# Kernel optimization log

Hardware: AMD Instinct MI355X
Metric: run time of the kernel (lower is better)

The kernel has to match this reference:

```python
import jax, jax.numpy as jnp
import numpy as np
import math

HEAD_SIZE = 64
BN_EPS = 1e-5  # BatchNorm eval with default running stats (mean=0, var=1)


def _rope_tables(seq_len, d):
    pos = jnp.arange(seq_len, dtype=jnp.float32)[:, None]
    div = jnp.exp(jnp.arange(0, d, 2, dtype=jnp.float32) * (-math.log(10000.0) / d))
    cos_pos = jnp.repeat(jnp.cos(pos * div), 2, axis=-1)  # [n, d]
    sin_pos = jnp.repeat(jnp.sin(pos * div), 2, axis=-1)  # [n, d]
    return cos_pos, sin_pos


def _rope(x, cos_pos, sin_pos):
    # interleaved rotation: (x0,x1) -> (-x1, x0)
    x2 = jnp.stack([-x[..., 1::2], x[..., ::2]], axis=-1).reshape(x.shape)
    return x * cos_pos + x2 * sin_pos


def _cbam(x, mlp_w1, mlp_b1, mlp_w2, mlp_b2, conv_w):
    # Channel gate: shared MLP over avg- and max-pooled [b, c] descriptors
    def mlp(v):
        return jax.nn.relu(v @ mlp_w1 + mlp_b1) @ mlp_w2 + mlp_b2
    avg = x.mean(axis=(2, 3))
    mx = x.max(axis=(2, 3))
    scale = jax.nn.sigmoid(mlp(avg) + mlp(mx))[:, :, None, None]
    x = x * scale
    # Spatial gate: 7x7 conv over channel-pooled (max, mean) maps
    comp = jnp.stack([x.max(axis=1), x.mean(axis=1)], axis=1)  # [b, 2, m, n]
    conv = jax.lax.conv_general_dilated(
        comp, conv_w, window_strides=(1, 1), padding=[(3, 3), (3, 3)],
        dimension_numbers=('NCHW', 'OIHW', 'NCHW'))
    conv = conv / jnp.sqrt(jnp.float32(1.0 + BN_EPS))  # identity BatchNorm (eval)
    return x * jax.nn.sigmoid(conv)


def setup_inputs() -> dict:
    key = jax.random.key(0)
    ks = jax.random.split(key, 12)
    b, n, h, c, d = 2, 512, 768, 108, HEAD_SIZE
    s = 0.02
    return {
        'inputs': jax.random.normal(ks[0], (b, n, h), jnp.float32),
        'event_inputs': jax.random.normal(ks[1], (c, h), jnp.float32),
        'mask': jnp.ones((b, n), jnp.int32),
        'w_dense': jax.random.normal(ks[2], (h, 2 * d), jnp.float32) * s,
        'b_dense': jax.random.normal(ks[3], (2 * d,), jnp.float32) * s,
        'w_event': jax.random.normal(ks[4], (h, d), jnp.float32) * s,
        'b_event': jax.random.normal(ks[5], (d,), jnp.float32) * s,
        'mlp_w1': jax.random.normal(ks[6], (c, c // 16), jnp.float32) * s,
        'mlp_b1': jax.random.normal(ks[7], (c // 16,), jnp.float32) * s,
        'mlp_w2': jax.random.normal(ks[8], (c // 16, c), jnp.float32) * s,
        'mlp_b2': jax.random.normal(ks[9], (c,), jnp.float32) * s,
        'conv_w': jax.random.normal(ks[10], (1, 2, 7, 7), jnp.float32) * s,
    }


def reference(inputs, event_inputs, mask, w_dense, b_dense, w_event, b_event,
              mlp_w1, mlp_b1, mlp_w2, mlp_b2, conv_w):
    b, n, _ = inputs.shape
    seq = inputs @ w_dense + b_dense          # [b, n, 2*d]
    ev = event_inputs @ w_event + b_event     # [c, d]
    qw, kw = seq[..., :HEAD_SIZE], seq[..., HEAD_SIZE:]
    cos_pos, sin_pos = _rope_tables(n, HEAD_SIZE)
    qw = _rope(qw, cos_pos, sin_pos)
    kw = _rope(kw, cos_pos, sin_pos)
    # event_output is broadcast over batch, so bcd collapses to cd
    logits = jnp.einsum('bmd,bnd,cd->bcmn', qw, kw, ev)
    logits = _cbam(logits, mlp_w1, mlp_b1, mlp_w2, mlp_b2, conv_w) + logits
    pad = (1 - mask).astype(bool)
    neg_inf = jnp.float32(-jnp.inf)
    logits = jnp.where(pad[:, None, :, None], neg_inf, logits)
    logits = jnp.where(pad[:, None, None, :], neg_inf, logits)
    tril_pen = jnp.tril(jnp.ones((n, n), logits.dtype), -1) * jnp.float32(1e12)
    logits = logits - tril_pen
    return logits / (HEAD_SIZE ** 0.5)
```

## Files before the change

kernel.cpp:

```cpp
#include <hip/hip_runtime.h>

constexpr int nB = 2;
constexpr int nS = 512;
constexpr int nH = 768;
constexpr int nC = 108;
constexpr int nD = 64;
constexpr int nBC = nB * nC;
constexpr long long nSS = (long long)nS * nS;

constexpr size_t QW_OFF    = 0;
constexpr size_t KW_OFF    = QW_OFF + (size_t)nB*nS*nD;
constexpr size_t EV_OFF    = KW_OFF + (size_t)nB*nS*nD;
constexpr size_t SUM_OFF   = EV_OFF + (size_t)nC*nD;
constexpr size_t MAX_OFF   = SUM_OFF + nBC;
constexpr size_t SCALE_OFF = MAX_OFF + nBC;
constexpr size_t COMP_OFF  = SCALE_OFF + nBC;
constexpr size_t SIG_OFF   = COMP_OFF + (size_t)nB*2*nS*nS;

typedef __attribute__((ext_vector_type(8))) short short8;
typedef __attribute__((ext_vector_type(4))) float f32x4;
union UFrag { uint4 u; short8 s; };

__device__ inline void atomicMaxF(float* addr, float v) {
    if (v >= 0.f) atomicMax((int*)addr, __float_as_int(v));
    else          atomicMin((unsigned int*)addr, __float_as_uint(v));
}

__device__ inline unsigned pack2bf(float a, float b) {
    unsigned ua = __float_as_uint(a), ub = __float_as_uint(b);
    ua = (ua + 0x7FFFu + ((ua >> 16) & 1u)) >> 16;
    ub = (ub + 0x7FFFu + ((ub >> 16) & 1u)) >> 16;
    return ua | (ub << 16);
}

__global__ __launch_bounds__(128) void k1_proj(
    const float* __restrict__ in, const float* __restrict__ evin,
    const float* __restrict__ wd, const float* __restrict__ bd,
    const float* __restrict__ we, const float* __restrict__ be,
    float* __restrict__ ws)
{
    __shared__ float rowS[nH];
    __shared__ float seqS[128];
    const int blk = blockIdx.x, tid = threadIdx.x;
    if (blk == 0 && tid < nBC) { ws[SUM_OFF + tid] = 0.f; ws[MAX_OFF + tid] = -INFINITY; }
    if (blk < nB * nS) {
        const int b = blk >> 9, m = blk & 511;
        const float* row = in + (size_t)blk * nH;
        for (int k = tid; k < nH; k += 128) rowS[k] = row[k];
        __syncthreads();
        float acc = bd[tid];
        for (int k = 0; k < nH; ++k) acc += rowS[k] * wd[k * 128 + tid];
        seqS[tid] = acc;
        __syncthreads();
        const int half = tid >> 6;
        const int j = tid & 63;
        const int p = j >> 1;
        const float div = expf(-0.28782313662425572f * (float)p);
        const float ang = (float)m * div;
        const float c = cosf(ang), s = sinf(ang);
        const float x0 = seqS[half * 64 + (j & ~1)];
        const float x1 = seqS[half * 64 + (j | 1)];
        const float v = (j & 1) ? (x1 * c + x0 * s) : (x0 * c - x1 * s);
        const size_t off = (half ? KW_OFF : QW_OFF) + ((size_t)(b * nS + m)) * nD + j;
        ws[off] = v;
    } else {
        const int ci = blk - nB * nS;
        const float* row = evin + (size_t)ci * nH;
        for (int k = tid; k < nH; k += 128) rowS[k] = row[k];
        __syncthreads();
        if (tid < nD) {
            float acc = be[tid];
            for (int k = 0; k < nH; ++k) acc += rowS[k] * we[k * nD + tid];
            ws[EV_OFF + (size_t)ci * nD + tid] = acc;
        }
    }
}


__device__ inline void stage_ev(const float* __restrict__ ws, uint4* evS, int tid) {
    for (int idx = tid; idx < 112 * 8; idx += 256) {
        const int row = idx >> 3, g = idx & 7;
        uint4 u = make_uint4(0, 0, 0, 0);
        if (row < nC) {
            const float* ep = ws + EV_OFF + row * nD + g * 8;
            float4 a = *(const float4*)ep;
            float4 b = *(const float4*)(ep + 4);
            u.x = pack2bf(a.x, a.y); u.y = pack2bf(a.z, a.w);
            u.z = pack2bf(b.x, b.y); u.w = pack2bf(b.z, b.w);
        }
        evS[row * 8 + (g ^ (row & 7))] = u;
    }
}

__device__ inline void stage_qk(const float* __restrict__ ws, float (*qkS)[68],
                                int b, int m0, int n0, int tid) {
    for (int idx = tid; idx < 64 * 16; idx += 256) {
        const int row = idx >> 4, d4 = (idx & 15) * 4;
        const float* src = (row < 32)
            ? (ws + QW_OFF + ((size_t)(b * nS + m0 + row)) * nD + d4)
            : (ws + KW_OFF + ((size_t)(b * nS + n0 + (row - 32))) * nD + d4);
        const float4 v = *(const float4*)src;
        qkS[row][d4 + 0] = v.x; qkS[row][d4 + 1] = v.y;
        qkS[row][d4 + 2] = v.z; qkS[row][d4 + 3] = v.w;
    }
}

__device__ inline void build_U(const float (*qkS)[68], uint4* U, int si, int sj, int tid) {
    const float* qr = qkS[si * 16 + (tid >> 4)];
    const float* kr = qkS[32 + sj * 16 + (tid & 15)];
#pragma unroll
    for (int g = 0; g < 8; ++g) {
        uint4 u;
        u.x = pack2bf(qr[g*8+0]*kr[g*8+0], qr[g*8+1]*kr[g*8+1]);
        u.y = pack2bf(qr[g*8+2]*kr[g*8+2], qr[g*8+3]*kr[g*8+3]);
        u.z = pack2bf(qr[g*8+4]*kr[g*8+4], qr[g*8+5]*kr[g*8+5]);
        u.w = pack2bf(qr[g*8+6]*kr[g*8+6], qr[g*8+7]*kr[g*8+7]);
        U[tid * 8 + (g ^ (tid & 7))] = u;
    }
}

__global__ __launch_bounds__(256) void kS_stats(float* __restrict__ ws)
{
    __shared__ uint4 evS[112 * 8];
    __shared__ uint4 U[256 * 8];
    __shared__ float qkS[64][68];
    __shared__ float sS[4][112], mS[4][112];

    const int tid = threadIdx.x;
    const int b = blockIdx.y;
    const int m0 = (blockIdx.x >> 4) * 32, n0 = (blockIdx.x & 15) * 32;
    const int lane = tid & 63, w = tid >> 6;
    const int fr = lane & 15, fg = lane >> 4;

    stage_ev(ws, evS, tid);
    stage_qk(ws, qkS, b, m0, n0, tid);

    float psum[28], pmax[28];
#pragma unroll
    for (int i = 0; i < 28; ++i) { psum[i] = 0.f; pmax[i] = -INFINITY; }

    for (int st = 0; st < 4; ++st) {
        __syncthreads();
        build_U(qkS, U, st >> 1, st & 1, tid);
        __syncthreads();

        short8 uf[4][2];
#pragma unroll
        for (int nf = 0; nf < 4; ++nf)
#pragma unroll
            for (int ks = 0; ks < 2; ++ks) {
                const int row = w * 64 + nf * 16 + fr;
                UFrag u; u.u = U[row * 8 + ((ks * 4 + fg) ^ (row & 7))];
                uf[nf][ks] = u.s;
            }
#pragma unroll
        for (int cf = 0; cf < 7; ++cf) {
            short8 ef[2];
#pragma unroll
            for (int ks = 0; ks < 2; ++ks) {
                const int row = cf * 16 + fr;
                UFrag u; u.u = evS[row * 8 + ((ks * 4 + fg) ^ (row & 7))];
                ef[ks] = u.s;
            }
            f32x4 acc[4] = {};
#pragma unroll
            for (int ks = 0; ks < 2; ++ks)
#pragma unroll
                for (int nf = 0; nf < 4; ++nf)
                    acc[nf] = __builtin_amdgcn_mfma_f32_16x16x32_bf16(ef[ks], uf[nf][ks], acc[nf], 0, 0, 0);
#pragma unroll
            for (int nf = 0; nf < 4; ++nf)
#pragma unroll
                for (int r = 0; r < 4; ++r) {
                    const float v = acc[nf][r];
                    psum[cf * 4 + r] += v;
                    pmax[cf * 4 + r] = fmaxf(pmax[cf * 4 + r], v);
                }
        }
    }

#pragma unroll
    for (int i = 0; i < 28; ++i) {
#pragma unroll
        for (int off = 1; off < 16; off <<= 1) {
            psum[i] += __shfl_xor(psum[i], off, 64);
            pmax[i] = fmaxf(pmax[i], __shfl_xor(pmax[i], off, 64));
        }
    }
    if (fr == 0) {
#pragma unroll
        for (int cf = 0; cf < 7; ++cf)
#pragma unroll
            for (int r = 0; r < 4; ++r) {
                const int c = cf * 16 + fg * 4 + r;
                sS[w][c] = psum[cf * 4 + r];
                mS[w][c] = pmax[cf * 4 + r];
            }
    }
    __syncthreads();
    if (tid < nC) {
        const float s = sS[0][tid] + sS[1][tid] + sS[2][tid] + sS[3][tid];
        const float mx = fmaxf(fmaxf(mS[0][tid], mS[1][tid]), fmaxf(mS[2][tid], mS[3][tid]));
        atomicAdd(&ws[SUM_OFF + b * nC + tid], s);
        atomicMaxF(&ws[MAX_OFF + b * nC + tid], mx);
    }
}

__global__ __launch_bounds__(256) void kC_comp(
    float* __restrict__ ws, const float* __restrict__ w1, const float* __restrict__ b1,
    const float* __restrict__ w2, const float* __restrict__ b2)
{
    __shared__ uint4 evS[112 * 8];
    __shared__ uint4 U[256 * 8];
    __shared__ float qkS[64][68];
    __shared__ float hS[12], scS[112];

    const int tid = threadIdx.x;
    const int b = blockIdx.y;
    const int m0 = (blockIdx.x >> 4) * 32, n0 = (blockIdx.x & 15) * 32;
    const int lane = tid & 63, w = tid >> 6;
    const int fr = lane & 15, fg = lane >> 4;

    if (tid < 12) {
        const int src = tid / 6, j = tid % 6;
        const float* v = ws + (src ? MAX_OFF : SUM_OFF) + b * nC;
        const float sc = src ? 1.f : (1.f / (float)nSS);
        float acc = b1[j];
        for (int cc = 0; cc < nC; ++cc) acc += v[cc] * sc * w1[cc * 6 + j];
        hS[tid] = fmaxf(acc, 0.f);
    }
    stage_ev(ws, evS, tid);
    stage_qk(ws, qkS, b, m0, n0, tid);
    __syncthreads();
    if (tid < 112) {
        float s = 0.f;
        if (tid < nC) {
            float acc = 2.f * b2[tid];
#pragma unroll
            for (int j = 0; j < 6; ++j) acc += (hS[j] + hS[6 + j]) * w2[j * nC + tid];
            s = 1.f / (1.f + expf(-acc));
            if (blockIdx.x == 0) ws[SCALE_OFF + b * nC + tid] = s;
        }
        scS[tid] = s;
    }

    for (int st = 0; st < 4; ++st) {
        const int si = st >> 1, sj = st & 1;
        __syncthreads();
        build_U(qkS, U, si, sj, tid);
        __syncthreads();

        short8 uf[4][2];
#pragma unroll
        for (int nf = 0; nf < 4; ++nf)
#pragma unroll
            for (int ks = 0; ks < 2; ++ks) {
                const int row = w * 64 + nf * 16 + fr;
                UFrag u; u.u = U[row * 8 + ((ks * 4 + fg) ^ (row & 7))];
                uf[nf][ks] = u.s;
            }
        float mx[4], sm[4];
#pragma unroll
        for (int nf = 0; nf < 4; ++nf) { mx[nf] = -INFINITY; sm[nf] = 0.f; }
#pragma unroll
        for (int cf = 0; cf < 7; ++cf) {
            short8 ef[2];
#pragma unroll
            for (int ks = 0; ks < 2; ++ks) {
                const int row = cf * 16 + fr;
                UFrag u; u.u = evS[row * 8 + ((ks * 4 + fg) ^ (row & 7))];
                ef[ks] = u.s;
            }
            f32x4 acc[4] = {};
#pragma unroll
            for (int ks = 0; ks < 2; ++ks)
#pragma unroll
                for (int nf = 0; nf < 4; ++nf)
                    acc[nf] = __builtin_amdgcn_mfma_f32_16x16x32_bf16(ef[ks], uf[nf][ks], acc[nf], 0, 0, 0);
            const bool valid = (cf < 6) || (fg < 3);
#pragma unroll
            for (int nf = 0; nf < 4; ++nf)
#pragma unroll
                for (int r = 0; r < 4; ++r) {
                    const float v = scS[cf * 16 + fg * 4 + r] * acc[nf][r];
                    sm[nf] += v;
                    if (valid) mx[nf] = fmaxf(mx[nf], v);
                }
        }
#pragma unroll
        for (int nf = 0; nf < 4; ++nf) {
            mx[nf] = fmaxf(mx[nf], __shfl_xor(mx[nf], 16, 64));
            mx[nf] = fmaxf(mx[nf], __shfl_xor(mx[nf], 32, 64));
            sm[nf] += __shfl_xor(sm[nf], 16, 64);
            sm[nf] += __shfl_xor(sm[nf], 32, 64);
        }
        if (fg == 0) {
#pragma unroll
            for (int nf = 0; nf < 4; ++nf) {
                const int m = m0 + si * 16 + 4 * w + nf;
                const int n = n0 + sj * 16 + fr;
                ws[COMP_OFF + (((size_t)(b * 2 + 0)) * nS + m) * nS + n] = mx[nf];
                ws[COMP_OFF + (((size_t)(b * 2 + 1)) * nS + m) * nS + n] = sm[nf] * (1.f / (float)nC);
            }
        }
    }
}

__global__ __launch_bounds__(512) void k5_conv(float* __restrict__ ws, const float* __restrict__ cw)
{
    __shared__ float S[14][520];
    __shared__ float wS[98];
    const int n = threadIdx.x;
    const int m = blockIdx.x & 511;
    const int b = blockIdx.x >> 9;
    if (n < 98) wS[n] = cw[n];
    for (int idx = n; idx < 14 * 518; idx += 512) {
        const int col = idx % 518;
        const int r = idx / 518;
        const int ch = r / 7, ky = r % 7;
        const int y = m + ky - 3;
        const int x = col - 3;
        float v = 0.f;
        if (y >= 0 && y < nS && x >= 0 && x < nS)
            v = ws[COMP_OFF + (((size_t)(b * 2 + ch)) * nS + y) * nS + x];
        S[r][col] = v;
    }
    __syncthreads();
    float acc = 0.f;
#pragma unroll
    for (int r = 0; r < 14; ++r)
#pragma unroll
        for (int kx = 0; kx < 7; ++kx)
            acc += S[r][n + kx] * wS[r * 7 + kx];
    acc *= 0.9999950000374997f;
    ws[SIG_OFF + ((size_t)b * nS + m) * nS + n] = 1.f / (1.f + expf(-acc));
}

__device__ inline void stage_tiles(const float* qwp, const float* kwp, const float* evp,
                                   uint4* ldsA, uint4* ldsB, int tid)
{
#pragma unroll
    for (int i = 0; i < 4; ++i) {
        const int q = tid + i * 256;
        const int row = q >> 3, g = q & 7;
        const int sw = row * 8 + (g ^ (row & 7));
        float4 x0 = *(const float4*)(qwp + row * nD + g * 8);
        float4 x1 = *(const float4*)(qwp + row * nD + g * 8 + 4);
        float4 e0 = *(const float4*)(evp + g * 8);
        float4 e1 = *(const float4*)(evp + g * 8 + 4);
        uint4 w;
        w.x = pack2bf(x0.x * e0.x, x0.y * e0.y);
        w.y = pack2bf(x0.z * e0.z, x0.w * e0.w);
        w.z = pack2bf(x1.x * e1.x, x1.y * e1.y);
        w.w = pack2bf(x1.z * e1.z, x1.w * e1.w);
        ldsA[sw] = w;
        float4 y0 = *(const float4*)(kwp + row * nD + g * 8);
        float4 y1 = *(const float4*)(kwp + row * nD + g * 8 + 4);
        uint4 v;
        v.x = pack2bf(y0.x, y0.y);
        v.y = pack2bf(y0.z, y0.w);
        v.z = pack2bf(y1.x, y1.y);
        v.w = pack2bf(y1.z, y1.w);
        ldsB[sw] = v;
    }
}

__device__ inline void mfma_tile(const uint4* ldsA, const uint4* ldsB,
                                 int wr, int wc, int fr, int fg, f32x4 acc[4][4])
{
#pragma unroll
    for (int ks = 0; ks < 2; ++ks) {
        short8 kf[4], qf[4];
#pragma unroll
        for (int i = 0; i < 4; ++i) {
            const int row = wc * 64 + i * 16 + fr;
            const int g = ks * 4 + fg;
            UFrag u; u.u = ldsB[row * 8 + (g ^ (row & 7))];
            kf[i] = u.s;
        }
#pragma unroll
        for (int j = 0; j < 4; ++j) {
            const int row = wr * 64 + j * 16 + fr;
            const int g = ks * 4 + fg;
            UFrag u; u.u = ldsA[row * 8 + (g ^ (row & 7))];
            qf[j] = u.s;
        }
#pragma unroll
        for (int i = 0; i < 4; ++i)
#pragma unroll
            for (int j = 0; j < 4; ++j)
                acc[i][j] = __builtin_amdgcn_mfma_f32_16x16x32_bf16(kf[i], qf[j], acc[i][j], 0, 0, 0);
    }
}

__global__ __launch_bounds__(256) void k6_final(
    float* __restrict__ ws, float* __restrict__ out, const int* __restrict__ mask)
{
    __shared__ uint4 ldsA[128 * 8];
    __shared__ uint4 ldsB[128 * 8];

    const int tid = threadIdx.x;
    const int mt = blockIdx.x >> 2, nt = blockIdx.x & 3;
    const int c  = blockIdx.y;
    const int b  = blockIdx.z;
    const int m0 = mt * 128, n0 = nt * 128;

    stage_tiles(ws + QW_OFF + ((size_t)(b * nS + m0)) * nD,
                ws + KW_OFF + ((size_t)(b * nS + n0)) * nD,
                ws + EV_OFF + (size_t)c * nD, ldsA, ldsB, tid);
    __syncthreads();

    const int lane = tid & 63;
    const int wv = tid >> 6;
    const int wr = wv >> 1, wc = wv & 1;
    const int fr = lane & 15, fg = lane >> 4;

    f32x4 acc[4][4] = {};
    mfma_tile(ldsA, ldsB, wr, wc, fr, fg, acc);

    const float scale = ws[SCALE_OFF + b * nC + c];
    const float* sig = ws + SIG_OFF + (size_t)b * nS * nS;
    float* outb = out + (size_t)(b * nC + c) * nSS;

#pragma unroll
    for (int i = 0; i < 4; ++i) {
#pragma unroll
        for (int j = 0; j < 4; ++j) {
            const int m = m0 + wr * 64 + j * 16 + fr;
            const int nb = n0 + wc * 64 + i * 16 + fg * 4;
            const float4 sg = *(const float4*)(sig + (size_t)m * nS + nb);
            const int mrow = mask[b * nS + m];
            const int4 mcol = *(const int4*)(mask + b * nS + nb);
            const f32x4 a = acc[i][j];
            float r[4];
            const float sgv[4] = { sg.x, sg.y, sg.z, sg.w };
            const int mcv[4] = { mcol.x, mcol.y, mcol.z, mcol.w };
#pragma unroll
            for (int rr = 0; rr < 4; ++rr) {
                float v = a[rr] * (1.f + scale * sgv[rr]);
                if (!mrow || !mcv[rr]) v = -INFINITY;
                if (m > nb + rr) v -= 1e12f;
                r[rr] = v * 0.125f;
            }
            *(float4*)(outb + (size_t)m * nS + nb) = make_float4(r[0], r[1], r[2], r[3]);
        }
    }
}

extern "C" void kernel_launch(void* const* d_in, const int* in_sizes, int n_in,
                              void* d_out, int out_size, void* d_ws, size_t ws_size,
                              hipStream_t stream)
{
    const float* inputs = (const float*)d_in[0];
    const float* evin   = (const float*)d_in[1];
    const int*   mask   = (const int*)d_in[2];
    const float* wd     = (const float*)d_in[3];
    const float* bd     = (const float*)d_in[4];
    const float* we     = (const float*)d_in[5];
    const float* be     = (const float*)d_in[6];
    const float* w1     = (const float*)d_in[7];
    const float* b1     = (const float*)d_in[8];
    const float* w2     = (const float*)d_in[9];
    const float* b2     = (const float*)d_in[10];
    const float* cw     = (const float*)d_in[11];
    float* out = (float*)d_out;
    float* ws  = (float*)d_ws;

    k1_proj<<<nB * nS + nC, 128, 0, stream>>>(inputs, evin, wd, bd, we, be, ws);
    kS_stats<<<dim3(256, nB), 256, 0, stream>>>(ws);
    kC_comp<<<dim3(256, nB), 256, 0, stream>>>(ws, w1, b1, w2, b2);
    k5_conv<<<nB * nS, 512, 0, stream>>>(ws, cw);
    k6_final<<<dim3(16, nC, nB), 256, 0, stream>>>(ws, out, mask);
}
```

Before: 172.2 us.

## Compute channel means algebraically and skip tril-masked tiles in conv and final

The channel average of the trilinear logits is now computed in closed form, as ev dotted with the product of summed q and k rows. The stats kernel therefore only tracks the max. The projection kernel now handles four rows per block and accumulates those q/k column sums atomically. The comp, conv and final kernels skip tiles strictly below the diagonal, where the 1e12 penalty dominates, and the final kernel writes a constant there. That constant drops CBAM terms which are negligible against the penalty, so it depends on float rounding of the huge offset.

New measurement: 170.1 us. Within noise of the previous version (-1.2%).

```diff
diff --git a/kernel.cpp b/kernel.cpp
--- a/kernel.cpp
+++ b/kernel.cpp
@@ -11,11 +11,11 @@
 constexpr size_t QW_OFF    = 0;
 constexpr size_t KW_OFF    = QW_OFF + (size_t)nB*nS*nD;
 constexpr size_t EV_OFF    = KW_OFF + (size_t)nB*nS*nD;
-constexpr size_t SUM_OFF   = EV_OFF + (size_t)nC*nD;
-constexpr size_t MAX_OFF   = SUM_OFF + nBC;
+constexpr size_t MAX_OFF   = EV_OFF + (size_t)nC*nD;
 constexpr size_t SCALE_OFF = MAX_OFF + nBC;
 constexpr size_t COMP_OFF  = SCALE_OFF + nBC;
 constexpr size_t SIG_OFF   = COMP_OFF + (size_t)nB*2*nS*nS;
+constexpr size_t SQK_OFF   = SIG_OFF;
 
 typedef __attribute__((ext_vector_type(8))) short short8;
 typedef __attribute__((ext_vector_type(4))) float f32x4;
@@ -33,49 +33,76 @@
     return ua | (ub << 16);
 }
 
-__global__ __launch_bounds__(128) void k1_proj(
+__global__ __launch_bounds__(256) void k1_proj(
     const float* __restrict__ in, const float* __restrict__ evin,
     const float* __restrict__ wd, const float* __restrict__ bd,
     const float* __restrict__ we, const float* __restrict__ be,
     float* __restrict__ ws)
 {
-    __shared__ float rowS[nH];
-    __shared__ float seqS[128];
+    __shared__ float rowT[nH][4];
+    __shared__ float accS[2][4][128];
+    __shared__ float ropeS[2][4][64];
     const int blk = blockIdx.x, tid = threadIdx.x;
-    if (blk == 0 && tid < nBC) { ws[SUM_OFF + tid] = 0.f; ws[MAX_OFF + tid] = -INFINITY; }
-    if (blk < nB * nS) {
-        const int b = blk >> 9, m = blk & 511;
-        const float* row = in + (size_t)blk * nH;
-        for (int k = tid; k < nH; k += 128) rowS[k] = row[k];
-        __syncthreads();
-        float acc = bd[tid];
-        for (int k = 0; k < nH; ++k) acc += rowS[k] * wd[k * 128 + tid];
-        seqS[tid] = acc;
-        __syncthreads();
-        const int half = tid >> 6;
-        const int j = tid & 63;
+    if (blk == 0 && tid < nBC) ws[MAX_OFF + tid] = -INFINITY;
+    if (blk < 256) {
+        const int b = blk >> 7;
+        const int m0 = (blk & 127) << 2;
+        const float* src = in + ((size_t)(b * nS + m0)) * nH;
+        for (int q = tid; q < 4 * nH; q += 256) {
+            const int r = q / nH, k = q - r * nH;
+            rowT[k][r] = src[q];
+        }
+        __syncthreads();
+        const int h = tid >> 7, c = tid & 127;
+        float a0 = h ? 0.f : bd[c], a1 = 0.f, a2 = 0.f, a3 = 0.f;
+        const float* wp = wd + (size_t)(h * 384) * 128 + c;
+        for (int k = h * 384; k < h * 384 + 384; ++k, wp += 128) {
+            const float w = *wp;
+            const float4 rv = *(const float4*)&rowT[k][0];
+            a0 += rv.x * w; a1 += rv.y * w; a2 += rv.z * w; a3 += rv.w * w;
+        }
+        accS[h][0][c] = a0; accS[h][1][c] = a1; accS[h][2][c] = a2; accS[h][3][c] = a3;
+        __syncthreads();
+        const int r = tid >> 6, j = tid & 63;
+        const int m = m0 + r;
         const int p = j >> 1;
         const float div = expf(-0.28782313662425572f * (float)p);
         const float ang = (float)m * div;
-        const float c = cosf(ang), s = sinf(ang);
-        const float x0 = seqS[half * 64 + (j & ~1)];
-        const float x1 = seqS[half * 64 + (j | 1)];
-        const float v = (j & 1) ? (x1 * c + x0 * s) : (x0 * c - x1 * s);
-        const size_t off = (half ? KW_OFF : QW_OFF) + ((size_t)(b * nS + m)) * nD + j;
-        ws[off] = v;
+        const float co = cosf(ang), si = sinf(ang);
+#pragma unroll
+        for (int half = 0; half < 2; ++half) {
+            const int i0 = half * 64 + (j & ~1);
+            const int i1 = half * 64 + (j | 1);
+            const float x0 = accS[0][r][i0] + accS[1][r][i0];
+            const float x1 = accS[0][r][i1] + accS[1][r][i1];
+            const float v = (j & 1) ? (x1 * co + x0 * si) : (x0 * co - x1 * si);
+            ws[(half ? KW_OFF : QW_OFF) + ((size_t)(b * nS + m)) * nD + j] = v;
+            ropeS[half][r][j] = v;
+        }
+        __syncthreads();
+        if (tid < 128) {
+            const int half = tid >> 6, jj = tid & 63;
+            const float t = ropeS[half][0][jj] + ropeS[half][1][jj]
+                          + ropeS[half][2][jj] + ropeS[half][3][jj];
+            atomicAdd(&ws[SQK_OFF + b * 128 + half * 64 + jj], t);
+        }
     } else {
-        const int ci = blk - nB * nS;
-        const float* row = evin + (size_t)ci * nH;
-        for (int k = tid; k < nH; k += 128) rowS[k] = row[k];
+        const int ci = blk - 256;
+        float* evrow = &rowT[0][0];
+        for (int k = tid; k < nH; k += 256) evrow[k] = evin[(size_t)ci * nH + k];
+        __syncthreads();
+        const int c = tid & 63, h = tid >> 6;
+        float acc = 0.f;
+        for (int k = h * 192; k < h * 192 + 192; ++k) acc += evrow[k] * we[k * nD + c];
+        accS[0][h][c] = acc;
         __syncthreads();
         if (tid < nD) {
-            float acc = be[tid];
-            for (int k = 0; k < nH; ++k) acc += rowS[k] * we[k * nD + tid];
-            ws[EV_OFF + (size_t)ci * nD + tid] = acc;
-        }
-    }
-}
-
+            const float s = be[tid] + accS[0][0][tid] + accS[0][1][tid]
+                          + accS[0][2][tid] + accS[0][3][tid];
+            ws[EV_OFF + (size_t)ci * nD + tid] = s;
+        }
+    }
+}
 
 __device__ inline void stage_ev(const float* __restrict__ ws, uint4* evS, int tid) {
     for (int idx = tid; idx < 112 * 8; idx += 256) {
@@ -124,7 +151,7 @@
     __shared__ uint4 evS[112 * 8];
     __shared__ uint4 U[256 * 8];
     __shared__ float qkS[64][68];
-    __shared__ float sS[4][112], mS[4][112];
+    __shared__ float mS[4][112];
 
     const int tid = threadIdx.x;
     const int b = blockIdx.y;
@@ -135,9 +162,9 @@
     stage_ev(ws, evS, tid);
     stage_qk(ws, qkS, b, m0, n0, tid);
 
-    float psum[28], pmax[28];
-#pragma unroll
-    for (int i = 0; i < 28; ++i) { psum[i] = 0.f; pmax[i] = -INFINITY; }
+    float pmax[28];
+#pragma unroll
+    for (int i = 0; i < 28; ++i) pmax[i] = -INFINITY;
 
     for (int st = 0; st < 4; ++st) {
         __syncthreads();
@@ -171,37 +198,27 @@
 #pragma unroll
             for (int nf = 0; nf < 4; ++nf)
 #pragma unroll
-                for (int r = 0; r < 4; ++r) {
-                    const float v = acc[nf][r];
-                    psum[cf * 4 + r] += v;
-                    pmax[cf * 4 + r] = fmaxf(pmax[cf * 4 + r], v);
-                }
+                for (int r = 0; r < 4; ++r)
+                    pmax[cf * 4 + r] = fmaxf(pmax[cf * 4 + r], acc[nf][r]);
         }
     }
 
 #pragma unroll
     for (int i = 0; i < 28; ++i) {
 #pragma unroll
-        for (int off = 1; off < 16; off <<= 1) {
-            psum[i] += __shfl_xor(psum[i], off, 64);
+        for (int off = 1; off < 16; off <<= 1)
             pmax[i] = fmaxf(pmax[i], __shfl_xor(pmax[i], off, 64));
-        }
     }
     if (fr == 0) {
 #pragma unroll
         for (int cf = 0; cf < 7; ++cf)
 #pragma unroll
-            for (int r = 0; r < 4; ++r) {
-                const int c = cf * 16 + fg * 4 + r;
-                sS[w][c] = psum[cf * 4 + r];
-                mS[w][c] = pmax[cf * 4 + r];
-            }
+            for (int r = 0; r < 4; ++r)
+                mS[w][cf * 16 + fg * 4 + r] = pmax[cf * 4 + r];
     }
     __syncthreads();
     if (tid < nC) {
-        const float s = sS[0][tid] + sS[1][tid] + sS[2][tid] + sS[3][tid];
         const float mx = fmaxf(fmaxf(mS[0][tid], mS[1][tid]), fmaxf(mS[2][tid], mS[3][tid]));
-        atomicAdd(&ws[SUM_OFF + b * nC + tid], s);
         atomicMaxF(&ws[MAX_OFF + b * nC + tid], mx);
     }
 }
@@ -214,23 +231,48 @@
     __shared__ uint4 U[256 * 8];
     __shared__ float qkS[64][68];
     __shared__ float hS[12], scS[112];
+    __shared__ float prodS[64], avgS[112];
 
     const int tid = threadIdx.x;
     const int b = blockIdx.y;
     const int m0 = (blockIdx.x >> 4) * 32, n0 = (blockIdx.x & 15) * 32;
+
+    {
+        const int mlo = m0 > 3 ? m0 - 3 : 0;
+        const int ncut = ((mlo >> 7) << 7) - 3;
+        if (n0 + 31 < ncut) return;
+    }
+
     const int lane = tid & 63, w = tid >> 6;
     const int fr = lane & 15, fg = lane >> 4;
 
+    if (tid < 64) {
+        const float sq = ws[SQK_OFF + b * 128 + tid];
+        const float sk = ws[SQK_OFF + b * 128 + 64 + tid];
+        prodS[tid] = sq * sk;
+    }
+    stage_ev(ws, evS, tid);
+    stage_qk(ws, qkS, b, m0, n0, tid);
+    __syncthreads();
+    if (tid < nC) {
+        const float* ep = ws + EV_OFF + (size_t)tid * nD;
+        float a = 0.f;
+#pragma unroll 8
+        for (int d = 0; d < nD; ++d) a += ep[d] * prodS[d];
+        avgS[tid] = a * (1.f / (float)nSS);
+    }
+    __syncthreads();
     if (tid < 12) {
         const int src = tid / 6, j = tid % 6;
-        const float* v = ws + (src ? MAX_OFF : SUM_OFF) + b * nC;
-        const float sc = src ? 1.f : (1.f / (float)nSS);
         float acc = b1[j];
-        for (int cc = 0; cc < nC; ++cc) acc += v[cc] * sc * w1[cc * 6 + j];
+        if (src == 0) {
+            for (int cc = 0; cc < nC; ++cc) acc += avgS[cc] * w1[cc * 6 + j];
+        } else {
+            const float* v = ws + MAX_OFF + b * nC;
+            for (int cc = 0; cc < nC; ++cc) acc += v[cc] * w1[cc * 6 + j];
+        }
         hS[tid] = fmaxf(acc, 0.f);
     }
-    stage_ev(ws, evS, tid);
-    stage_qk(ws, qkS, b, m0, n0, tid);
     __syncthreads();
     if (tid < 112) {
         float s = 0.f;
@@ -313,6 +355,7 @@
     const int n = threadIdx.x;
     const int m = blockIdx.x & 511;
     const int b = blockIdx.x >> 9;
+    const int n0q = (m >> 7) << 7;
     if (n < 98) wS[n] = cw[n];
     for (int idx = n; idx < 14 * 518; idx += 512) {
         const int col = idx % 518;
@@ -321,19 +364,21 @@
         const int y = m + ky - 3;
         const int x = col - 3;
         float v = 0.f;
-        if (y >= 0 && y < nS && x >= 0 && x < nS)
+        if (y >= 0 && y < nS && x >= n0q - 3 && x < nS)
             v = ws[COMP_OFF + (((size_t)(b * 2 + ch)) * nS + y) * nS + x];
         S[r][col] = v;
     }
     __syncthreads();
-    float acc = 0.f;
-#pragma unroll
-    for (int r = 0; r < 14; ++r)
-#pragma unroll
-        for (int kx = 0; kx < 7; ++kx)
-            acc += S[r][n + kx] * wS[r * 7 + kx];
-    acc *= 0.9999950000374997f;
-    ws[SIG_OFF + ((size_t)b * nS + m) * nS + n] = 1.f / (1.f + expf(-acc));
+    if (n >= n0q) {
+        float acc = 0.f;
+#pragma unroll
+        for (int r = 0; r < 14; ++r)
+#pragma unroll
+            for (int kx = 0; kx < 7; ++kx)
+                acc += S[r][n + kx] * wS[r * 7 + kx];
+        acc *= 0.9999950000374997f;
+        ws[SIG_OFF + ((size_t)b * nS + m) * nS + n] = 1.f / (1.f + expf(-acc));
+    }
 }
 
 __device__ inline void stage_tiles(const float* qwp, const float* kwp, const float* evp,
@@ -404,6 +449,26 @@
     const int c  = blockIdx.y;
     const int b  = blockIdx.z;
     const int m0 = mt * 128, n0 = nt * 128;
+    float* outb = out + (size_t)(b * nC + c) * nSS;
+
+    if (mt > nt) {
+        const float CF = -1e12f * 0.125f;
+        const int rr0 = tid >> 5;
+        const int nn = n0 + (tid & 31) * 4;
+        const int4 mc = *(const int4*)(mask + b * nS + nn);
+#pragma unroll
+        for (int p = 0; p < 16; ++p) {
+            const int m = m0 + p * 8 + rr0;
+            const int mr = mask[b * nS + m];
+            float4 v;
+            v.x = (mr && mc.x) ? CF : -INFINITY;
+            v.y = (mr && mc.y) ? CF : -INFINITY;
+            v.z = (mr && mc.z) ? CF : -INFINITY;
+            v.w = (mr && mc.w) ? CF : -INFINITY;
+            *(float4*)(outb + (size_t)m * nS + nn) = v;
+        }
+        return;
+    }
 
     stage_tiles(ws + QW_OFF + ((size_t)(b * nS + m0)) * nD,
                 ws + KW_OFF + ((size_t)(b * nS + n0)) * nD,
@@ -420,7 +485,6 @@
 
     const float scale = ws[SCALE_OFF + b * nC + c];
     const float* sig = ws + SIG_OFF + (size_t)b * nS * nS;
-    float* outb = out + (size_t)(b * nC + c) * nSS;
 
 #pragma unroll
     for (int i = 0; i < 4; ++i) {
@@ -466,7 +530,8 @@
     float* out = (float*)d_out;
     float* ws  = (float*)d_ws;
 
-    k1_proj<<<nB * nS + nC, 128, 0, stream>>>(inputs, evin, wd, bd, we, be, ws);
+    hipMemsetAsync((char*)d_ws + SQK_OFF * sizeof(float), 0, 256 * sizeof(float), stream);
+    k1_proj<<<256 + nC, 256, 0, stream>>>(inputs, evin, wd, bd, we, be, ws);
     kS_stats<<<dim3(256, nB), 256, 0, stream>>>(ws);
     kC_comp<<<dim3(256, nB), 256, 0, stream>>>(ws, w1, b1, w2, b2);
     k5_conv<<<nB * nS, 512, 0, stream>>>(ws, cw);
```
